# Kernel tuning notes

Measured on AMD Instinct MI355X. Metric: run time of the kernel, lower is better.

The kernel has to match this reference:

```python
import jax, jax.numpy as jnp
import numpy as np


def setup_inputs() -> dict:
    key = jax.random.key(0)
    k1, k2 = jax.random.split(key)
    B, S, D, E = 4, 4096, 2048, 64
    x = jax.random.normal(k1, (B, S, D), dtype=jnp.float32)
    gate_w = jax.random.normal(k2, (E, D), dtype=jnp.float32) * (1.0 / np.sqrt(D))
    return {"x": x, "gate_w": gate_w, "top_k": 2}


def reference(x, gate_w, top_k):
    # logits = x @ W^T : [B, S, E]
    logits = jnp.einsum("bsd,ed->bse", x, gate_w)
    probs = jax.nn.softmax(logits, axis=-1)
    top_k_probs, top_k_indices = jax.lax.top_k(probs, top_k)
    top_k_probs = top_k_probs / jnp.sum(top_k_probs, axis=-1, keepdims=True)
    return (top_k_probs, top_k_indices, probs)
```

## Files before the change

### kernel.cpp

```cpp
#include <hip/hip_runtime.h>
#include <math.h>


typedef _Float16 half8  __attribute__((ext_vector_type(8)));
typedef float    floatx4 __attribute__((ext_vector_type(4)));

#define NTOK  16384
#define DDIM  2048
#define NE    64
#define TPB   64
#define NSTEP 32

__device__ inline void split8(const float4& a, const float4& b,
                              half8& hi, half8& lo) {
    float f[8] = {a.x, a.y, a.z, a.w, b.x, b.y, b.z, b.w};
#pragma unroll
    for (int j = 0; j < 8; ++j) {
        const _Float16 h = (_Float16)f[j];
        hi[j] = h;
        lo[j] = (_Float16)(f[j] - (float)h);
    }
}

__global__ __launch_bounds__(256) void w_split(const float* __restrict__ W,
                                               _Float16* __restrict__ img) {
    const int idx  = blockIdx.x * 256 + threadIdx.x;
    const int step = idx >> 10;
    const int u    = idx & 1023;
    const int hl   = u >> 9;
    const int v    = u & 511;
    const int e    = v >> 3, g = v & 7;
    const float* src = W + (size_t)e * DDIM + step * 64 + 8 * (g ^ (e & 7));
    const float4 a = *(const float4*)(src);
    const float4 b = *(const float4*)(src + 4);
    half8 hi, lo;
    split8(a, b, hi, lo);
    *(half8*)(img + (size_t)idx * 8) = (hl == 0) ? hi : lo;
}

__global__ __launch_bounds__(512) void router_mfma(
    const float* __restrict__ x,
    const _Float16* __restrict__ img,
    float* __restrict__ out)
{
    __shared__ __align__(16) float tiles[16384];
    __shared__ __align__(16) float lg[TPB * 68];

    const int tid = threadIdx.x;
    const int L   = tid & 63;
    const int wv  = __builtin_amdgcn_readfirstlane(tid >> 6);
    const int kh  = wv & 1;
    const int nh  = (wv >> 1) & 1;
    const int mh  = wv >> 2;
    const int c   = L & 15, q = L >> 4;
    const int tok0 = blockIdx.x * TPB;

    const int gfrag = (q + 4 * kh) ^ (L & 7);
    int aoff[2], boff[2];
#pragma unroll
    for (int mt = 0; mt < 2; ++mt)
        aoff[mt] = ((mh * 32 + mt * 16 + c) * 8 + gfrag) * 8;
#pragma unroll
    for (int nt = 0; nt < 2; ++nt)
        boff[nt] = ((nh * 32 + nt * 16 + c) * 8 + gfrag) * 8;

    const int sr = tid >> 3, so = tid & 7;
    const float* xsrc = x + (size_t)(tok0 + sr) * DDIM + 8 * (so ^ (sr & 7));
    const int    xdst = (sr * 8 + so) * 8;
    const float* wsrc = (const float*)img;

    floatx4 acc[2][2];
#pragma unroll
    for (int i = 0; i < 2; ++i)
#pragma unroll
        for (int j = 0; j < 2; ++j) acc[i][j] = (floatx4)0.f;

    auto stage = [&](int sel, const float4& xa, const float4& xb,
                     const float4& wh4, const float4& wl4) {
        _Float16* nb = (_Float16*)&tiles[sel * 8192];
        half8 hi, lo; split8(xa, xb, hi, lo);
        *(half8*)(nb + xdst)        = hi;
        *(half8*)(nb + 4096 + xdst) = lo;
        *(float4*)(nb + 8192  + tid * 8) = wh4;
        *(float4*)(nb + 12288 + tid * 8) = wl4;
    };

    auto compute = [&](int sel) {
        const _Float16* base = (const _Float16*)&tiles[sel * 8192];
        const _Float16* xh = base;
        const _Float16* xl = base + 4096;
        const _Float16* wh = base + 8192;
        const _Float16* wl = base + 12288;

        half8 Ah[2], Al[2], Bh[2], Bl[2];
#pragma unroll
        for (int mt = 0; mt < 2; ++mt) {
            Ah[mt] = *(const half8*)(xh + aoff[mt]);
            Al[mt] = *(const half8*)(xl + aoff[mt]);
        }
#pragma unroll
        for (int nt = 0; nt < 2; ++nt) {
            Bh[nt] = *(const half8*)(wh + boff[nt]);
            Bl[nt] = *(const half8*)(wl + boff[nt]);
        }
#pragma unroll
        for (int mt = 0; mt < 2; ++mt)
#pragma unroll
            for (int nt = 0; nt < 2; ++nt) {
                acc[mt][nt] = __builtin_amdgcn_mfma_f32_16x16x32_f16(Ah[mt], Bh[nt], acc[mt][nt], 0, 0, 0);
                acc[mt][nt] = __builtin_amdgcn_mfma_f32_16x16x32_f16(Al[mt], Bh[nt], acc[mt][nt], 0, 0, 0);
                acc[mt][nt] = __builtin_amdgcn_mfma_f32_16x16x32_f16(Ah[mt], Bl[nt], acc[mt][nt], 0, 0, 0);
            }
    };

    float4 pxa, pxb, pwh, pwl;
    {
        const float4 xa  = *(const float4*)(xsrc);
        const float4 xb  = *(const float4*)(xsrc + 4);
        const float4 wh4 = *(const float4*)(wsrc + (size_t)tid * 4);
        const float4 wl4 = *(const float4*)(wsrc + (size_t)(512 + tid) * 4);
        pxa = *(const float4*)(xsrc + 64);
        pxb = *(const float4*)(xsrc + 68);
        pwh = *(const float4*)(wsrc + (size_t)(1024 + tid) * 4);
        pwl = *(const float4*)(wsrc + (size_t)(1536 + tid) * 4);
        stage(0, xa, xb, wh4, wl4);
    }
    __syncthreads();

#pragma unroll 2
    for (int t = 0; t < NSTEP - 2; ++t) {
        const float4 nxa = *(const float4*)(xsrc + (t + 2) * 64);
        const float4 nxb = *(const float4*)(xsrc + (t + 2) * 64 + 4);
        const float4 nwh = *(const float4*)(wsrc + (size_t)((t + 2) * 1024 + tid) * 4);
        const float4 nwl = *(const float4*)(wsrc + (size_t)((t + 2) * 1024 + 512 + tid) * 4);

        compute(t & 1);
        stage((t + 1) & 1, pxa, pxb, pwh, pwl);
        __syncthreads();

        pxa = nxa; pxb = nxb; pwh = nwh; pwl = nwl;
    }

    compute((NSTEP - 2) & 1);
    stage((NSTEP - 1) & 1, pxa, pxb, pwh, pwl);
    __syncthreads();
    compute((NSTEP - 1) & 1);
    __syncthreads();

    float* exch = tiles;
    const int p = wv >> 1;
    if (kh == 1) {
        float* e0 = &exch[(p * 64 + L) * 20];
        *(float4*)(e0 + 0)  = make_float4(acc[0][0][0], acc[0][0][1], acc[0][0][2], acc[0][0][3]);
        *(float4*)(e0 + 4)  = make_float4(acc[0][1][0], acc[0][1][1], acc[0][1][2], acc[0][1][3]);
        *(float4*)(e0 + 8)  = make_float4(acc[1][0][0], acc[1][0][1], acc[1][0][2], acc[1][0][3]);
        *(float4*)(e0 + 12) = make_float4(acc[1][1][0], acc[1][1][1], acc[1][1][2], acc[1][1][3]);
    }
    __syncthreads();
    if (kh == 0) {
        const float* e0 = &exch[(p * 64 + L) * 20];
        float4 v;
        v = *(const float4*)(e0 + 0);  acc[0][0][0] += v.x; acc[0][0][1] += v.y; acc[0][0][2] += v.z; acc[0][0][3] += v.w;
        v = *(const float4*)(e0 + 4);  acc[0][1][0] += v.x; acc[0][1][1] += v.y; acc[0][1][2] += v.z; acc[0][1][3] += v.w;
        v = *(const float4*)(e0 + 8);  acc[1][0][0] += v.x; acc[1][0][1] += v.y; acc[1][0][2] += v.z; acc[1][0][3] += v.w;
        v = *(const float4*)(e0 + 12); acc[1][1][0] += v.x; acc[1][1][1] += v.y; acc[1][1][2] += v.z; acc[1][1][3] += v.w;
#pragma unroll
        for (int mt = 0; mt < 2; ++mt)
#pragma unroll
            for (int nt = 0; nt < 2; ++nt)
#pragma unroll
                for (int r = 0; r < 4; ++r)
                    lg[(mh * 32 + mt * 16 + q * 4 + r) * 68 + nh * 32 + nt * 16 + c] = acc[mt][nt][r];
    }
    __syncthreads();

    if (tid < 64) {
        const int token = tok0 + tid;
        float* row = &lg[tid * 68];
        float pr[NE];
#pragma unroll
        for (int e = 0; e < NE; ++e) pr[e] = row[e];

        float m = pr[0];
#pragma unroll
        for (int e = 1; e < NE; ++e) m = fmaxf(m, pr[e]);
        float s = 0.f;
#pragma unroll
        for (int e = 0; e < NE; ++e) { pr[e] = expf(pr[e] - m); s += pr[e]; }
        const float inv = 1.f / s;

        float v1 = -1.f; int i1 = 0;
#pragma unroll
        for (int e = 0; e < NE; ++e) { if (pr[e] > v1) { v1 = pr[e]; i1 = e; } }
        float v2 = -1.f; int i2 = 0;
#pragma unroll
        for (int e = 0; e < NE; ++e) { if (e != i1 && pr[e] > v2) { v2 = pr[e]; i2 = e; } }

        const float ts = v1 + v2;
        float* out_tp = out;
        float* out_ti = out + 2 * NTOK;
        *(float2*)(out_tp + token * 2) = make_float2(v1 / ts, v2 / ts);
        *(float2*)(out_ti + token * 2) = make_float2((float)i1, (float)i2);

#pragma unroll
        for (int e = 0; e < NE; ++e) row[e] = pr[e] * inv;
    }
    __syncthreads();

    {
        float* out_p = out + 4 * NTOK + (size_t)tok0 * NE;
#pragma unroll
        for (int i = 0; i < 2; ++i) {
            const int f = tid + 512 * i;
            const int r = f >> 4, c4 = f & 15;
            const float4 v = *(const float4*)&lg[r * 68 + 4 * c4];
            *(float4*)(out_p + f * 4) = v;
        }
    }
}

extern "C" void kernel_launch(void* const* d_in, const int* in_sizes, int n_in,
                              void* d_out, int out_size, void* d_ws, size_t ws_size,
                              hipStream_t stream) {
    const float* x = (const float*)d_in[0];
    const float* W = (const float*)d_in[1];
    float* out     = (float*)d_out;
    _Float16* img  = (_Float16*)d_ws;

    w_split<<<dim3(128), dim3(256), 0, stream>>>(W, img);
    router_mfma<<<dim3(NTOK / TPB), dim3(512), 0, stream>>>(x, img, out);
}
```

Baseline: 205.4 us.

## Halve router token tile and stream weights directly into LDS asynchronously

Tokens per block drop from 64 to 32 and each block now has 256 threads with two blocks per CU. The split-fp16 weight tiles are copied global-to-LDS with global_load_lds instead of going through registers. The main loop becomes a single double-buffered loop with explicit vmcnt waits and raw s_barrier. The intent is to cut register pressure, raise occupancy and overlap weight fetches with MFMA work. The cost is that each block reloads the full weight image for half as many tokens, which doubles weight traffic through L2.

```diff
diff --git a/kernel.cpp b/kernel.cpp
--- a/kernel.cpp
+++ b/kernel.cpp
@@ -8,7 +8,7 @@
 #define NTOK  16384
 #define DDIM  2048
 #define NE    64
-#define TPB   64
+#define TPB   32
 #define NSTEP 32
 
 __device__ inline void split8(const float4& a, const float4& b,
@@ -20,6 +20,13 @@
         hi[j] = h;
         lo[j] = (_Float16)(f[j] - (float)h);
     }
+}
+
+typedef const __attribute__((address_space(1))) unsigned int* as1_u32p;
+typedef __attribute__((address_space(3))) unsigned int*       as3_u32p;
+
+__device__ inline void gload_lds16(const void* g, void* l) {
+    __builtin_amdgcn_global_load_lds((as1_u32p)g, (as3_u32p)l, 16, 0, 0);
 }
 
 __global__ __launch_bounds__(256) void w_split(const float* __restrict__ W,
@@ -38,20 +45,19 @@
     *(half8*)(img + (size_t)idx * 8) = (hl == 0) ? hi : lo;
 }
 
-__global__ __launch_bounds__(512) void router_mfma(
+__global__ __launch_bounds__(256, 2) void router_mfma(
     const float* __restrict__ x,
     const _Float16* __restrict__ img,
     float* __restrict__ out)
 {
-    __shared__ __align__(16) float tiles[16384];
+    __shared__ __align__(16) _Float16 tiles[2 * 12288];
     __shared__ __align__(16) float lg[TPB * 68];
 
     const int tid = threadIdx.x;
     const int L   = tid & 63;
     const int wv  = __builtin_amdgcn_readfirstlane(tid >> 6);
     const int kh  = wv & 1;
-    const int nh  = (wv >> 1) & 1;
-    const int mh  = wv >> 2;
+    const int nh  = wv >> 1;
     const int c   = L & 15, q = L >> 4;
     const int tok0 = blockIdx.x * TPB;
 
@@ -59,7 +65,7 @@
     int aoff[2], boff[2];
 #pragma unroll
     for (int mt = 0; mt < 2; ++mt)
-        aoff[mt] = ((mh * 32 + mt * 16 + c) * 8 + gfrag) * 8;
+        aoff[mt] = ((mt * 16 + c) * 8 + gfrag) * 8;
 #pragma unroll
     for (int nt = 0; nt < 2; ++nt)
         boff[nt] = ((nh * 32 + nt * 16 + c) * 8 + gfrag) * 8;
@@ -67,7 +73,6 @@
     const int sr = tid >> 3, so = tid & 7;
     const float* xsrc = x + (size_t)(tok0 + sr) * DDIM + 8 * (so ^ (sr & 7));
     const int    xdst = (sr * 8 + so) * 8;
-    const float* wsrc = (const float*)img;
 
     floatx4 acc[2][2];
 #pragma unroll
@@ -75,22 +80,29 @@
 #pragma unroll
         for (int j = 0; j < 2; ++j) acc[i][j] = (floatx4)0.f;
 
-    auto stage = [&](int sel, const float4& xa, const float4& xb,
-                     const float4& wh4, const float4& wl4) {
-        _Float16* nb = (_Float16*)&tiles[sel * 8192];
+    auto stage_w = [&](int sel, int t) {
+        const char* src = (const char*)img + (size_t)t * 16384;
+#pragma unroll
+        for (int r = 0; r < 4; ++r) {
+            const int gi0 = r * 256 + wv * 64;
+            gload_lds16(src + (size_t)(gi0 + L) * 16,
+                        &tiles[sel * 12288 + 4096 + gi0 * 8]);
+        }
+    };
+
+    auto stage_x = [&](int sel, const float4& xa, const float4& xb) {
+        _Float16* nb = &tiles[sel * 12288];
         half8 hi, lo; split8(xa, xb, hi, lo);
         *(half8*)(nb + xdst)        = hi;
-        *(half8*)(nb + 4096 + xdst) = lo;
-        *(float4*)(nb + 8192  + tid * 8) = wh4;
-        *(float4*)(nb + 12288 + tid * 8) = wl4;
+        *(half8*)(nb + 2048 + xdst) = lo;
     };
 
     auto compute = [&](int sel) {
-        const _Float16* base = (const _Float16*)&tiles[sel * 8192];
+        const _Float16* base = &tiles[sel * 12288];
         const _Float16* xh = base;
-        const _Float16* xl = base + 4096;
-        const _Float16* wh = base + 8192;
-        const _Float16* wl = base + 12288;
+        const _Float16* xl = base + 2048;
+        const _Float16* wh = base + 4096;
+        const _Float16* wl = base + 8192;
 
         half8 Ah[2], Al[2], Bh[2], Bl[2];
 #pragma unroll
@@ -113,42 +125,46 @@
             }
     };
 
-    float4 pxa, pxb, pwh, pwl;
+    float4 pxa, pxb;
     {
-        const float4 xa  = *(const float4*)(xsrc);
-        const float4 xb  = *(const float4*)(xsrc + 4);
-        const float4 wh4 = *(const float4*)(wsrc + (size_t)tid * 4);
-        const float4 wl4 = *(const float4*)(wsrc + (size_t)(512 + tid) * 4);
+        stage_w(0, 0);
+        __builtin_amdgcn_sched_barrier(0);
+        const float4 xa = *(const float4*)(xsrc);
+        const float4 xb = *(const float4*)(xsrc + 4);
+        __builtin_amdgcn_sched_barrier(0);
         pxa = *(const float4*)(xsrc + 64);
         pxb = *(const float4*)(xsrc + 68);
-        pwh = *(const float4*)(wsrc + (size_t)(1024 + tid) * 4);
-        pwl = *(const float4*)(wsrc + (size_t)(1536 + tid) * 4);
-        stage(0, xa, xb, wh4, wl4);
-    }
-    __syncthreads();
-
-#pragma unroll 2
-    for (int t = 0; t < NSTEP - 2; ++t) {
-        const float4 nxa = *(const float4*)(xsrc + (t + 2) * 64);
-        const float4 nxb = *(const float4*)(xsrc + (t + 2) * 64 + 4);
-        const float4 nwh = *(const float4*)(wsrc + (size_t)((t + 2) * 1024 + tid) * 4);
-        const float4 nwl = *(const float4*)(wsrc + (size_t)((t + 2) * 1024 + 512 + tid) * 4);
-
+        __builtin_amdgcn_sched_barrier(0);
+        stage_x(0, xa, xb);
+        asm volatile("s_waitcnt vmcnt(2) lgkmcnt(0)" ::: "memory");
+        __builtin_amdgcn_sched_barrier(0);
+        __builtin_amdgcn_s_barrier();
+    }
+
+    for (int t = 0; t < NSTEP - 1; ++t) {
+        stage_w((t + 1) & 1, t + 1);
+        __builtin_amdgcn_sched_barrier(0);
+        float4 nxa = pxa, nxb = pxb;
+        if (t + 2 < NSTEP) {
+            nxa = *(const float4*)(xsrc + (t + 2) * 64);
+            nxb = *(const float4*)(xsrc + (t + 2) * 64 + 4);
+        }
+        __builtin_amdgcn_sched_barrier(0);
         compute(t & 1);
-        stage((t + 1) & 1, pxa, pxb, pwh, pwl);
-        __syncthreads();
-
-        pxa = nxa; pxb = nxb; pwh = nwh; pwl = nwl;
-    }
-
-    compute((NSTEP - 2) & 1);
-    stage((NSTEP - 1) & 1, pxa, pxb, pwh, pwl);
-    __syncthreads();
+        stage_x((t + 1) & 1, pxa, pxb);
+        if (t + 2 < NSTEP)
+            asm volatile("s_waitcnt vmcnt(2) lgkmcnt(0)" ::: "memory");
+        else
+            asm volatile("s_waitcnt vmcnt(0) lgkmcnt(0)" ::: "memory");
+        __builtin_amdgcn_sched_barrier(0);
+        __builtin_amdgcn_s_barrier();
+        pxa = nxa; pxb = nxb;
+    }
     compute((NSTEP - 1) & 1);
     __syncthreads();
 
-    float* exch = tiles;
-    const int p = wv >> 1;
+    float* exch = (float*)tiles;
+    const int p = nh;
     if (kh == 1) {
         float* e0 = &exch[(p * 64 + L) * 20];
         *(float4*)(e0 + 0)  = make_float4(acc[0][0][0], acc[0][0][1], acc[0][0][2], acc[0][0][3]);
@@ -170,11 +186,11 @@
             for (int nt = 0; nt < 2; ++nt)
 #pragma unroll
                 for (int r = 0; r < 4; ++r)
-                    lg[(mh * 32 + mt * 16 + q * 4 + r) * 68 + nh * 32 + nt * 16 + c] = acc[mt][nt][r];
-    }
-    __syncthreads();
-
-    if (tid < 64) {
+                    lg[(mt * 16 + q * 4 + r) * 68 + nh * 32 + nt * 16 + c] = acc[mt][nt][r];
+    }
+    __syncthreads();
+
+    if (tid < TPB) {
         const int token = tok0 + tid;
         float* row = &lg[tid * 68];
         float pr[NE];
@@ -211,7 +227,7 @@
         float* out_p = out + 4 * NTOK + (size_t)tok0 * NE;
 #pragma unroll
         for (int i = 0; i < 2; ++i) {
-            const int f = tid + 512 * i;
+            const int f = tid + 256 * i;
             const int r = f >> 4, c4 = f & 15;
             const float4 v = *(const float4*)&lg[r * 68 + 4 * c4];
             *(float4*)(out_p + f * 4) = v;
@@ -228,5 +244,5 @@
     _Float16* img  = (_Float16*)d_ws;
 
     w_split<<<dim3(128), dim3(256), 0, stream>>>(W, img);
-    router_mfma<<<dim3(NTOK / TPB), dim3(512), 0, stream>>>(x, img, out);
-}
+    router_mfma<<<dim3(NTOK / TPB), dim3(256), 0, stream>>>(x, img, out);
+}
```

New measurement: 209.3 us. About the same (+1.9%).
